# Kernel tuning notes

Hardware: AMD Instinct MI355X
Metric: run time of the kernel (lower is better)

Reference implementation:

```python
import jax, jax.numpy as jnp
import numpy as np

N, E, B = 50000, 800000, 64
F_IN, HID, H, L = 128, 128, 4, 4
C = HID // H  # per-head channels = 32
NEG_SLOPE = 0.2  # PyG GATConv default leaky_relu slope


def setup_inputs() -> dict:
    key = jax.random.key(0)
    ks = iter(jax.random.split(key, 32))
    rn = lambda shape, s=0.05: jax.random.normal(next(ks), shape, jnp.float32) * s
    x = jax.random.normal(next(ks), (N, F_IN), jnp.float32)
    edge_index = jax.random.randint(next(ks), (2, E), 0, N, jnp.int32)
    edge_attr = jax.random.uniform(next(ks), (E, 2), dtype=jnp.float32)
    batch = jnp.sort(jax.random.randint(next(ks), (N,), 0, B, jnp.int32))
    return {
        "x": x, "edge_attr": edge_attr,
        "Win": rn((F_IN, HID)), "b_in": jnp.zeros((HID,), jnp.float32),
        "We1": rn((2, 16)), "be1": jnp.zeros((16,), jnp.float32),
        "We2": rn((16, H)), "be2": jnp.zeros((H,), jnp.float32),
        "Wl": rn((L, HID, HID)), "a_src": rn((L, H, C)), "a_dst": rn((L, H, C)),
        "bl": jnp.zeros((L, HID), jnp.float32),
        "ln_g": jnp.ones((L, HID), jnp.float32), "ln_b": jnp.zeros((L, HID), jnp.float32),
        "Wg1": rn((HID, HID // 2)), "bg1": jnp.zeros((HID // 2,), jnp.float32),
        "Wg2": rn((HID // 2, 1)), "bg2": jnp.zeros((1,), jnp.float32),
        "edge_index": edge_index, "batch": batch,
    }


def _layer_norm(x, g, b, eps=1e-5):
    mu = x.mean(-1, keepdims=True)
    var = ((x - mu) ** 2).mean(-1, keepdims=True)
    return (x - mu) * jax.lax.rsqrt(var + eps) * g + b


def _gat_conv(h, src, dst, W, a_s, a_d, bias):
    # PyG GATConv (shared lin for src/dst), add_self_loops already in src/dst.
    xp = (h @ W).reshape(N, H, C)            # [N,H,C]
    as_n = (xp * a_s).sum(-1)                # [N,H]
    ad_n = (xp * a_d).sum(-1)                # [N,H]
    e = jax.nn.leaky_relu(as_n[src] + ad_n[dst], NEG_SLOPE)   # [E+N,H]
    m = jax.ops.segment_max(e, dst, num_segments=N)           # stable softmax per dst
    p = jnp.exp(e - m[dst])
    s = jax.ops.segment_sum(p, dst, num_segments=N)
    alpha = p / (s[dst] + 1e-16)
    out = jax.ops.segment_sum(xp[src] * alpha[..., None], dst, num_segments=N)
    return out.reshape(N, HID) + bias


def reference(x, edge_attr, Win, b_in, We1, be1, We2, be2, Wl, a_src, a_dst, bl,
              ln_g, ln_b, Wg1, bg1, Wg2, bg2, edge_index, batch):
    h = x @ Win + b_in                                   # input_proj
    # edge bias MLP -> per-edge scalar -> scatter_add crit_signal (no self loops)
    edge_bias = jax.nn.relu(edge_attr @ We1 + be1) @ We2 + be2   # [E,H]
    edge_scalar = edge_bias.mean(axis=1)                         # [E]
    crit = jnp.zeros((N,), h.dtype).at[edge_index[1]].add(edge_scalar)[:, None]
    # self loops for GATConv
    loop = jnp.arange(N, dtype=edge_index.dtype)
    src = jnp.concatenate([edge_index[0], loop])
    dst = jnp.concatenate([edge_index[1], loop])
    for i in range(L):  # fixed small layer count
        h_new = _gat_conv(h, src, dst, Wl[i], a_src[i], a_dst[i], bl[i])
        h_new = _layer_norm(h_new, ln_g[i], ln_b[i])
        h_new = h_new + crit                             # broadcast [N,1]
        h = h_new + h                                    # residual (shapes match); dropout=eval noop
    # GlobalAttention pooling: softmax(gate) over each graph, weighted sum
    gate = jnp.tanh(h @ Wg1 + bg1) @ Wg2 + bg2           # [N,1]
    gmax = jax.ops.segment_max(gate, batch, num_segments=B)
    gp = jnp.exp(gate - gmax[batch])
    gs = jax.ops.segment_sum(gp, batch, num_segments=B)
    gate_sm = gp / (gs[batch] + 1e-16)
    return jax.ops.segment_sum(gate_sm * h, batch, num_segments=B)   # [B,HID]
```

## Files before the change

kernel.cpp:

```cpp
#include <hip/hip_runtime.h>
#include <math.h>

#define N_NODES 50000
#define N_EDGES 800000
#define N_B     64

typedef __attribute__((ext_vector_type(8))) short v8s;
typedef __attribute__((ext_vector_type(4))) float v4f;
typedef __attribute__((ext_vector_type(2))) float v2f;

__device__ __forceinline__ float lrelu(float x){ return x > 0.f ? x : 0.2f*x; }
__device__ __forceinline__ unsigned short f2b(float f){
  unsigned u = __float_as_uint(f);
  return (unsigned short)((u + 0x7fffu + ((u >> 16) & 1u)) >> 16);
}
__device__ __forceinline__ float blo(unsigned u){ return __uint_as_float(u << 16); }
__device__ __forceinline__ float bhi(unsigned u){ return __uint_as_float(u & 0xffff0000u); }

__global__ void k_convsetup(const float* __restrict__ Win, const float* __restrict__ Wl,
                            const float* __restrict__ a_src, const float* __restrict__ a_dst,
                            const float* __restrict__ Wg1, const int* __restrict__ batch,
                            unsigned short* __restrict__ WinT, unsigned short* __restrict__ WlT,
                            unsigned short* __restrict__ Wg1T, int* __restrict__ start,
                            int* __restrict__ cnt){
  if (blockIdx.x >= 384){
    int i = (blockIdx.x - 384)*256 + threadIdx.x;
    if (i >= N_NODES) return;
    cnt[i] = 0;
    int b = batch[i];
    int bp = (i == 0) ? -1 : batch[i-1];
    for (int j = bp+1; j <= b; j++) start[j] = i;
    if (i == N_NODES-1){
      for (int j = b+1; j <= N_B; j++) start[j] = N_NODES;
    }
    return;
  }
  int i = blockIdx.x*256 + threadIdx.x;
  if (i < 16384){
    int n = i >> 7, k = i & 127;
    WinT[n*128+k] = f2b(Win[k*128+n]);
    return;
  }
  i -= 16384;
  if (i < 65536){
    int l = i >> 14, n = (i >> 7) & 127, k = i & 127;
    WlT[l*144*128 + n*128 + k] = f2b(Wl[l*16384 + k*128 + n]);
    return;
  }
  i -= 65536;
  if (i < 4096){
    int l = i >> 10, k = (i >> 3) & 127, t = i & 7;
    int hh = t & 3, sd = t >> 2;
    const float* av = (sd ? a_dst : a_src) + l*128 + hh*32;
    const float* wr = Wl + l*16384 + k*128 + hh*32;
    float s = 0.f;
    #pragma unroll
    for (int c = 0; c < 32; c++) s = fmaf(wr[c], av[c], s);
    WlT[l*144*128 + (128 + sd*4 + hh)*128 + k] = f2b(s);
    return;
  }
  i -= 4096;
  if (i < 4096){
    int l = i >> 10, r = (i >> 7) & 7, k = i & 127;
    WlT[l*144*128 + (136+r)*128 + k] = 0;
    return;
  }
  i -= 4096;
  if (i < 8192){
    int n = i >> 7, k = i & 127;
    Wg1T[n*128+k] = f2b(Wg1[k*64+n]);
  }
}

__global__ void k_hist(const int* __restrict__ ei, int* __restrict__ cnt, int* __restrict__ rank){
  int t = blockIdx.x*256 + threadIdx.x;
  if (t >= 200000) return;
  #pragma unroll
  for (int r = 0; r < 4; r++){
    int e = t + r*200000;
    int d = ei[N_EDGES + e];
    rank[e] = atomicAdd(&cnt[d], 1);
  }
}

__global__ void k_scan1(const int* __restrict__ cnt, int* __restrict__ incl, int* __restrict__ part){
  __shared__ int sh[256];
  int tid = threadIdx.x, i = blockIdx.x*256 + tid;
  int v = (i < N_NODES) ? cnt[i] : 0;
  sh[tid] = v; __syncthreads();
  for (int off = 1; off < 256; off <<= 1){
    int t = (tid >= off) ? sh[tid-off] : 0;
    __syncthreads();
    sh[tid] += t; __syncthreads();
  }
  if (i < N_NODES) incl[i] = sh[tid];
  if (tid == 255) part[blockIdx.x] = sh[255];
}
__global__ void k_scan23(const int* __restrict__ cnt, const int* __restrict__ incl,
                         const int* __restrict__ part, int* __restrict__ off){
  __shared__ int red[4];
  __shared__ int bsum;
  int tid = threadIdx.x, lane = tid & 63, wave = tid >> 6;
  int v = (tid < (int)blockIdx.x) ? part[tid] : 0;
  #pragma unroll
  for (int m = 1; m < 64; m <<= 1) v += __shfl_xor(v, m);
  if (lane == 0) red[wave] = v;
  __syncthreads();
  if (tid == 0) bsum = red[0]+red[1]+red[2]+red[3];
  __syncthreads();
  int i = blockIdx.x*256 + tid;
  if (i >= N_NODES) return;
  int e = incl[i] - cnt[i] + bsum;
  off[i] = e;
  if (i == N_NODES-1) off[N_NODES] = e + cnt[i];
}

__global__ void k_fill(const float* __restrict__ ea, const float* __restrict__ We1,
                       const float* __restrict__ be1, const float* __restrict__ We2,
                       const float* __restrict__ be2, const int* __restrict__ ei,
                       const int* __restrict__ off, const int* __restrict__ rank,
                       int2* __restrict__ es){
  __shared__ float w0[16], w1[16], bb[16], w2s[16];
  __shared__ float b2s;
  int tid = threadIdx.x;
  if (tid < 16){
    w0[tid] = We1[tid]; w1[tid] = We1[16+tid]; bb[tid] = be1[tid];
    w2s[tid] = 0.25f*(We2[tid*4]+We2[tid*4+1]+We2[tid*4+2]+We2[tid*4+3]);
  }
  if (tid == 0) b2s = 0.25f*(be2[0]+be2[1]+be2[2]+be2[3]);
  __syncthreads();
  int t = blockIdx.x*256 + tid;
  if (t >= 200000) return;
  #pragma unroll
  for (int r = 0; r < 4; r++){
    int e = t + r*200000;
    float a0 = ea[2*e], a1 = ea[2*e+1];
    float s = b2s;
    #pragma unroll
    for (int j = 0; j < 16; j++){
      float v = fmaf(a0, w0[j], fmaf(a1, w1[j], bb[j]));
      v = v > 0.f ? v : 0.f;
      s = fmaf(v, w2s[j], s);
    }
    int d = ei[N_EDGES + e];
    int p = off[d] + rank[e];
    es[p] = make_int2(ei[e], __float_as_int(s));
  }
}

template<int NT, int MODE>
__global__ __launch_bounds__(256) void k_mgemm(
    const float* __restrict__ A, const unsigned short* __restrict__ Bt,
    const float* __restrict__ bias,
    float* __restrict__ h,
    unsigned short* __restrict__ xpb, float* __restrict__ asn, float* __restrict__ adn,
    const float* __restrict__ Wg2, const float* __restrict__ bg2, float* __restrict__ gate)
{
  __shared__ __attribute__((aligned(16))) unsigned short Bs[NT*16][136];
  __shared__ __attribute__((aligned(16))) unsigned short As[4][16][136];
  int tid = threadIdx.x, wave = tid >> 6, lane = tid & 63;
  int l15 = lane & 15, quad = lane >> 4;
  int rbase = blockIdx.x * 64;
  for (int id = tid; id < NT*16*16; id += 256){
    int r = id >> 4, ch = id & 15;
    *(v8s*)&Bs[r][ch*8] = *(const v8s*)(Bt + r*128 + ch*8);
  }
  for (int id = tid; id < 64*16; id += 256){
    int r = id >> 4, ch = id & 15;
    int gr = rbase + r;
    v8s v = {0,0,0,0,0,0,0,0};
    if (gr < N_NODES){
      const float* Af = A + (size_t)gr*128 + ch*8;
      float4 va = *(const float4*)Af;
      float4 vb = *(const float4*)(Af + 4);
      v[0]=(short)f2b(va.x); v[1]=(short)f2b(va.y); v[2]=(short)f2b(va.z); v[3]=(short)f2b(va.w);
      v[4]=(short)f2b(vb.x); v[5]=(short)f2b(vb.y); v[6]=(short)f2b(vb.z); v[7]=(short)f2b(vb.w);
    }
    *(v8s*)&As[r >> 4][r & 15][ch*8] = v;
  }
  __syncthreads();
  v4f acc[NT];
  #pragma unroll
  for (int t = 0; t < NT; t++) acc[t] = (v4f){0.f,0.f,0.f,0.f};
  #pragma unroll
  for (int kb = 0; kb < 4; kb++){
    v8s a = *(v8s*)&As[wave][l15][kb*32 + quad*8];
    #pragma unroll
    for (int ct = 0; ct < NT; ct++){
      v8s b = *(v8s*)&Bs[ct*16 + l15][kb*32 + quad*8];
      acc[ct] = __builtin_amdgcn_mfma_f32_16x16x32_bf16(a, b, acc[ct], 0, 0, 0);
    }
  }
  int row0 = rbase + wave*16 + quad*4;
  if (MODE == 0){
    #pragma unroll
    for (int ct = 0; ct < 8; ct++){
      float bcol = bias[ct*16 + l15];
      #pragma unroll
      for (int r = 0; r < 4; r++){
        int gr = row0 + r;
        if (gr < N_NODES) h[(size_t)gr*128 + ct*16 + l15] = acc[ct][r] + bcol;
      }
    }
  } else if (MODE == 1){
    #pragma unroll
    for (int ct = 0; ct < 8; ct++){
      #pragma unroll
      for (int r = 0; r < 4; r++){
        int gr = row0 + r;
        if (gr < N_NODES) xpb[(size_t)gr*128 + ct*16 + l15] = f2b(acc[ct][r]);
      }
    }
    #pragma unroll
    for (int r = 0; r < 4; r++){
      int gr = row0 + r;
      if (gr < N_NODES){
        float v = acc[NT-1][r];
        if (l15 < 4) asn[gr*4 + l15] = v;
        else if (l15 < 8) adn[gr*4 + (l15-4)] = v;
      }
    }
  } else {
    float part[4] = {0.f,0.f,0.f,0.f};
    #pragma unroll
    for (int ct = 0; ct < NT; ct++){
      float b1 = bias[ct*16 + l15];
      float w2 = Wg2[ct*16 + l15];
      #pragma unroll
      for (int r = 0; r < 4; r++) part[r] = fmaf(tanhf(acc[ct][r] + b1), w2, part[r]);
    }
    #pragma unroll
    for (int m = 1; m < 16; m <<= 1){
      #pragma unroll
      for (int r = 0; r < 4; r++) part[r] += __shfl_xor(part[r], m);
    }
    if (l15 == 0){
      float b2 = bg2[0];
      #pragma unroll
      for (int r = 0; r < 4; r++){
        int gr = row0 + r;
        if (gr < N_NODES) gate[gr] = part[r] + b2;
      }
    }
  }
}

template<bool CRIT>
__global__ __launch_bounds__(256) void k_aggr(
    const unsigned short* __restrict__ xpb, const float* __restrict__ asn,
    const float* __restrict__ adn, const int* __restrict__ off,
    const int2* __restrict__ es,
    const float* __restrict__ bl, const float* __restrict__ lng,
    const float* __restrict__ lnb, float* __restrict__ crit,
    float* __restrict__ h)
{
  __shared__ float lp[4][256];
  int wave = threadIdx.x >> 6, lane = threadIdx.x & 63;
  int n = blockIdx.x*4 + wave;
  if (n >= N_NODES) return;
  int base = off[n], deg = off[n+1] - base;
  float4 ad4 = *(const float4*)(adn + n*4);
  float4 asf = *(const float4*)(asn + n*4);
  float ex = lrelu(asf.x+ad4.x), ey = lrelu(asf.y+ad4.y);
  float ez = lrelu(asf.z+ad4.z), ew = lrelu(asf.w+ad4.w);
  const unsigned* xw = (const unsigned*)xpb;
  float* myp = &lp[wave][0];
  int hh = lane >> 4;
  float cr, dsum = 0.f;
  v2f acc;
  unsigned us = (xw + ((size_t)(unsigned)n << 6))[lane];
  acc.x = blo(us); acc.y = bhi(us);

  if (deg <= 64){
    int sreg = 0;
    float cw = 0.f;
    float p0 = 0.f, p1 = 0.f, p2 = 0.f, p3 = 0.f;
    if (lane < deg){
      int2 er = es[base + lane];
      sreg = er.x;
      float4 a = *(const float4*)(asn + sreg*4);
      p0 = __expf(lrelu(a.x+ad4.x) - ex);
      p1 = __expf(lrelu(a.y+ad4.y) - ey);
      p2 = __expf(lrelu(a.z+ad4.z) - ez);
      p3 = __expf(lrelu(a.w+ad4.w) - ew);
      if (CRIT) cw = __int_as_float(er.y);
    }
    if (CRIT){
      #pragma unroll
      for (int m = 1; m < 64; m <<= 1) cw += __shfl_xor(cw, m);
      if (lane == 0) crit[n] = cw;
      cr = cw;
    } else cr = crit[n];
    *(float4*)(&myp[4*lane]) = make_float4(p0,p1,p2,p3);
    __threadfence_block();
    int degR = (deg + 7) & ~7;
    for (int c = 0; c < degR; c += 8){
      unsigned u[8];
      #pragma unroll
      for (int k = 0; k < 8; k++){
        int s0 = __builtin_amdgcn_readlane(sreg, c + k);
        u[k] = (xw + ((size_t)(unsigned)s0 << 6))[lane];
      }
      #pragma unroll
      for (int k = 0; k < 8; k++){
        float q = myp[4*(c+k) + hh];
        dsum += q;
        v2f v = {blo(u[k]), bhi(u[k])};
        acc += q * v;
      }
    }
    __threadfence_block();
  } else {
    if (CRIT){
      float cw = 0.f;
      for (int j = lane; j < deg; j += 64) cw += __int_as_float(es[base + j].y);
      #pragma unroll
      for (int m = 1; m < 64; m <<= 1) cw += __shfl_xor(cw, m);
      if (lane == 0) crit[n] = cw;
      cr = cw;
    } else cr = crit[n];
    for (int j0 = 0; j0 < deg; j0 += 64){
      int clen = deg - j0; if (clen > 64) clen = 64;
      int sreg = 0;
      float p0 = 0.f, p1 = 0.f, p2 = 0.f, p3 = 0.f;
      if (lane < clen){
        sreg = es[base + j0 + lane].x;
        float4 a = *(const float4*)(asn + sreg*4);
        p0 = __expf(lrelu(a.x+ad4.x) - ex);
        p1 = __expf(lrelu(a.y+ad4.y) - ey);
        p2 = __expf(lrelu(a.z+ad4.z) - ez);
        p3 = __expf(lrelu(a.w+ad4.w) - ew);
      }
      *(float4*)(&myp[4*lane]) = make_float4(p0,p1,p2,p3);
      __threadfence_block();
      int clenR = (clen + 7) & ~7;
      for (int c = 0; c < clenR; c += 8){
        unsigned u[8];
        #pragma unroll
        for (int k = 0; k < 8; k++){
          int s0 = __builtin_amdgcn_readlane(sreg, c + k);
          u[k] = (xw + ((size_t)(unsigned)s0 << 6))[lane];
        }
        #pragma unroll
        for (int k = 0; k < 8; k++){
          float q = myp[4*(c+k) + hh];
          dsum += q;
          v2f v = {blo(u[k]), bhi(u[k])};
          acc += q * v;
        }
      }
      __threadfence_block();
    }
  }
  float rden = 1.f / (dsum + 1.f + 1e-16f);
  int c0 = 2*lane;
  float2 blv = *(const float2*)(bl + c0);
  float o0 = acc.x*rden + blv.x;
  float o1 = acc.y*rden + blv.y;
  float su = o0 + o1, sq = o0*o0 + o1*o1;
  #pragma unroll
  for (int m = 1; m < 64; m <<= 1){ su += __shfl_xor(su, m); sq += __shfl_xor(sq, m); }
  float mu  = su * (1.f/128.f);
  float var = sq * (1.f/128.f) - mu*mu; var = var > 0.f ? var : 0.f;
  float inv = rsqrtf(var + 1e-5f);
  float2 rv  = *(const float2*)(h + (size_t)n*128 + c0);
  float2 gv  = *(const float2*)(lng + c0);
  float2 bv2 = *(const float2*)(lnb + c0);
  o0 = (o0-mu)*inv*gv.x + bv2.x + cr + rv.x;
  o1 = (o1-mu)*inv*gv.y + bv2.y + cr + rv.y;
  *(float2*)(&h[(size_t)n*128 + c0]) = make_float2(o0, o1);
}

__global__ __launch_bounds__(256) void k_pool(
    const float* __restrict__ h, float* __restrict__ gate,
    const int* __restrict__ start, float* __restrict__ out)
{
  __shared__ float red[4];
  __shared__ float sbc;
  __shared__ float4 accs[8][32];
  int b = blockIdx.x;
  int s0 = start[b], s1 = start[b+1];
  int tid = threadIdx.x, lane = tid & 63, wave = tid >> 6;
  float m = -3.0e38f;
  for (int i = s0 + tid; i < s1; i += 256) m = fmaxf(m, gate[i]);
  #pragma unroll
  for (int k = 1; k < 64; k <<= 1) m = fmaxf(m, __shfl_xor(m, k));
  if (lane == 0) red[wave] = m;
  __syncthreads();
  if (tid == 0) sbc = fmaxf(fmaxf(red[0],red[1]), fmaxf(red[2],red[3]));
  __syncthreads();
  float gm = sbc;
  __syncthreads();
  float s = 0.f;
  for (int i = s0 + tid; i < s1; i += 256){
    float p = __expf(gate[i] - gm);
    gate[i] = p;
    s += p;
  }
  #pragma unroll
  for (int k = 1; k < 64; k <<= 1) s += __shfl_xor(s, k);
  if (lane == 0) red[wave] = s;
  __syncthreads();
  if (tid == 0) sbc = red[0]+red[1]+red[2]+red[3];
  __syncthreads();
  float inv = 1.f / (sbc + 1e-16f);
  int c4 = (tid & 31) * 4;
  int g  = tid >> 5;
  float4 acc = make_float4(0.f,0.f,0.f,0.f);
  for (int i = s0 + g; i < s1; i += 8){
    float p = gate[i];
    float4 hv = *(const float4*)(h + (size_t)i*128 + c4);
    acc.x = fmaf(p,hv.x,acc.x); acc.y = fmaf(p,hv.y,acc.y);
    acc.z = fmaf(p,hv.z,acc.z); acc.w = fmaf(p,hv.w,acc.w);
  }
  accs[g][tid & 31] = acc;
  __syncthreads();
  if (g == 0){
    float4 t = acc;
    #pragma unroll
    for (int k = 1; k < 8; k++){
      float4 o = accs[k][tid & 31];
      t.x += o.x; t.y += o.y; t.z += o.z; t.w += o.w;
    }
    t.x *= inv; t.y *= inv; t.z *= inv; t.w *= inv;
    *(float4*)(out + b*128 + c4) = t;
  }
}

extern "C" void kernel_launch(void* const* d_in, const int* in_sizes, int n_in,
                              void* d_out, int out_size, void* d_ws, size_t ws_size,
                              hipStream_t stream){
  (void)in_sizes; (void)n_in; (void)out_size; (void)ws_size;
  const float* x    = (const float*)d_in[0];
  const float* ea   = (const float*)d_in[1];
  const float* Win  = (const float*)d_in[2];
  const float* b_in = (const float*)d_in[3];
  const float* We1  = (const float*)d_in[4];
  const float* be1  = (const float*)d_in[5];
  const float* We2  = (const float*)d_in[6];
  const float* be2  = (const float*)d_in[7];
  const float* Wl   = (const float*)d_in[8];
  const float* a_src= (const float*)d_in[9];
  const float* a_dst= (const float*)d_in[10];
  const float* bl   = (const float*)d_in[11];
  const float* lng  = (const float*)d_in[12];
  const float* lnb  = (const float*)d_in[13];
  const float* Wg1  = (const float*)d_in[14];
  const float* bg1  = (const float*)d_in[15];
  const float* Wg2  = (const float*)d_in[16];
  const float* bg2  = (const float*)d_in[17];
  const int*   ei   = (const int*)d_in[18];
  const int*   batch= (const int*)d_in[19];
  float* out = (float*)d_out;

  char* w = (char*)d_ws;
  auto alloc = [&](size_t bytes){ char* p = w; w += (bytes + 255) & ~(size_t)255; return p; };
  float* h    = (float*)alloc((size_t)N_NODES*128*4);
  unsigned short* xpb = (unsigned short*)alloc((size_t)N_NODES*128*2);
  float* asn  = (float*)alloc((size_t)N_NODES*4*4);
  float* adn  = (float*)alloc((size_t)N_NODES*4*4);
  float* crit = (float*)alloc((size_t)N_NODES*4);
  int*   cnt  = (int*)alloc((size_t)N_NODES*4);
  int*   incl = (int*)alloc((size_t)N_NODES*4);
  int*   part = (int*)alloc(256*4);
  int*   off  = (int*)alloc((size_t)(N_NODES+1)*4);
  int*   rank = (int*)alloc((size_t)N_EDGES*4);
  int2*  es   = (int2*)alloc((size_t)N_EDGES*8);
  float* gate = (float*)alloc((size_t)N_NODES*4);
  int*   start= (int*)alloc((size_t)(N_B+1)*4);
  unsigned short* WinT = (unsigned short*)alloc((size_t)128*128*2);
  unsigned short* WlT  = (unsigned short*)alloc((size_t)4*144*128*2);
  unsigned short* Wg1T = (unsigned short*)alloc((size_t)64*128*2);

  int nb_n = (N_NODES + 255)/256;
  int nb_w = (N_NODES + 3)/4;
  int nb_g = (N_NODES + 63)/64;
  int nb_cs = 384 + nb_n;
  int nb_4e = (200000 + 255)/256;

  k_convsetup<<<nb_cs,256,0,stream>>>(Win, Wl, a_src, a_dst, Wg1, batch,
                                      WinT, WlT, Wg1T, start, cnt);
  k_hist<<<nb_4e,256,0,stream>>>(ei, cnt, rank);
  k_mgemm<8,0><<<nb_g,256,0,stream>>>(x, WinT, b_in, h,
                                      nullptr, nullptr, nullptr, nullptr, nullptr, nullptr);
  k_scan1<<<nb_n,256,0,stream>>>(cnt, incl, part);
  k_scan23<<<nb_n,256,0,stream>>>(cnt, incl, part, off);
  k_fill<<<nb_4e,256,0,stream>>>(ea, We1, be1, We2, be2, ei, off, rank, es);
  for (int l = 0; l < 4; l++){
    k_mgemm<9,1><<<nb_g,256,0,stream>>>(h, WlT + (size_t)l*144*128, nullptr, nullptr,
                                        xpb, asn, adn, nullptr, nullptr, nullptr);
    if (l == 0)
      k_aggr<true><<<nb_w,256,0,stream>>>(xpb, asn, adn, off, es,
                                          bl + l*128, lng + l*128, lnb + l*128, crit, h);
    else
      k_aggr<false><<<nb_w,256,0,stream>>>(xpb, asn, adn, off, es,
                                           bl + l*128, lng + l*128, lnb + l*128, crit, h);
  }
  k_mgemm<4,2><<<nb_g,256,0,stream>>>(h, Wg1T, bg1, nullptr,
                                      nullptr, nullptr, nullptr, Wg2, bg2, gate);
  k_pool<<<N_B,256,0,stream>>>(h, gate, start, out);
}
```

Baseline: 440.1 us.

## Split pooling across four blocks per graph, widen edge loops and gather batches

```diff
diff --git a/kernel.cpp b/kernel.cpp
--- a/kernel.cpp
+++ b/kernel.cpp
@@ -22,11 +22,12 @@
                             const float* __restrict__ Wg1, const int* __restrict__ batch,
                             unsigned short* __restrict__ WinT, unsigned short* __restrict__ WlT,
                             unsigned short* __restrict__ Wg1T, int* __restrict__ start,
-                            int* __restrict__ cnt){
+                            int* __restrict__ cnt, float* __restrict__ out){
   if (blockIdx.x >= 384){
     int i = (blockIdx.x - 384)*256 + threadIdx.x;
     if (i >= N_NODES) return;
     cnt[i] = 0;
+    if (i < N_B*128) out[i] = 0.f;
     int b = batch[i];
     int bp = (i == 0) ? -1 : batch[i-1];
     for (int j = bp+1; j <= b; j++) start[j] = i;
@@ -74,10 +75,10 @@
 
 __global__ void k_hist(const int* __restrict__ ei, int* __restrict__ cnt, int* __restrict__ rank){
   int t = blockIdx.x*256 + threadIdx.x;
-  if (t >= 200000) return;
-  #pragma unroll
-  for (int r = 0; r < 4; r++){
-    int e = t + r*200000;
+  if (t >= 100000) return;
+  #pragma unroll
+  for (int r = 0; r < 8; r++){
+    int e = t + r*100000;
     int d = ei[N_EDGES + e];
     rank[e] = atomicAdd(&cnt[d], 1);
   }
@@ -130,10 +131,10 @@
   if (tid == 0) b2s = 0.25f*(be2[0]+be2[1]+be2[2]+be2[3]);
   __syncthreads();
   int t = blockIdx.x*256 + tid;
-  if (t >= 200000) return;
-  #pragma unroll
-  for (int r = 0; r < 4; r++){
-    int e = t + r*200000;
+  if (t >= 100000) return;
+  #pragma unroll
+  for (int r = 0; r < 8; r++){
+    int e = t + r*100000;
     float a0 = ea[2*e], a1 = ea[2*e+1];
     float s = b2s;
     #pragma unroll
@@ -293,16 +294,16 @@
     } else cr = crit[n];
     *(float4*)(&myp[4*lane]) = make_float4(p0,p1,p2,p3);
     __threadfence_block();
-    int degR = (deg + 7) & ~7;
-    for (int c = 0; c < degR; c += 8){
-      unsigned u[8];
-      #pragma unroll
-      for (int k = 0; k < 8; k++){
+    int degR = ((deg + 11) / 12) * 12;
+    for (int c = 0; c < degR; c += 12){
+      unsigned u[12];
+      #pragma unroll
+      for (int k = 0; k < 12; k++){
         int s0 = __builtin_amdgcn_readlane(sreg, c + k);
         u[k] = (xw + ((size_t)(unsigned)s0 << 6))[lane];
       }
       #pragma unroll
-      for (int k = 0; k < 8; k++){
+      for (int k = 0; k < 12; k++){
         float q = myp[4*(c+k) + hh];
         dsum += q;
         v2f v = {blo(u[k]), bhi(u[k])};
@@ -372,13 +373,13 @@
 }
 
 __global__ __launch_bounds__(256) void k_pool(
-    const float* __restrict__ h, float* __restrict__ gate,
+    const float* __restrict__ h, const float* __restrict__ gate,
     const int* __restrict__ start, float* __restrict__ out)
 {
   __shared__ float red[4];
   __shared__ float sbc;
   __shared__ float4 accs[8][32];
-  int b = blockIdx.x;
+  int b = blockIdx.x >> 2, quarter = blockIdx.x & 3;
   int s0 = start[b], s1 = start[b+1];
   int tid = threadIdx.x, lane = tid & 63, wave = tid >> 6;
   float m = -3.0e38f;
@@ -392,11 +393,7 @@
   float gm = sbc;
   __syncthreads();
   float s = 0.f;
-  for (int i = s0 + tid; i < s1; i += 256){
-    float p = __expf(gate[i] - gm);
-    gate[i] = p;
-    s += p;
-  }
+  for (int i = s0 + tid; i < s1; i += 256) s += __expf(gate[i] - gm);
   #pragma unroll
   for (int k = 1; k < 64; k <<= 1) s += __shfl_xor(s, k);
   if (lane == 0) red[wave] = s;
@@ -407,8 +404,8 @@
   int c4 = (tid & 31) * 4;
   int g  = tid >> 5;
   float4 acc = make_float4(0.f,0.f,0.f,0.f);
-  for (int i = s0 + g; i < s1; i += 8){
-    float p = gate[i];
+  for (int i = s0 + quarter*8 + g; i < s1; i += 32){
+    float p = __expf(gate[i] - gm);
     float4 hv = *(const float4*)(h + (size_t)i*128 + c4);
     acc.x = fmaf(p,hv.x,acc.x); acc.y = fmaf(p,hv.y,acc.y);
     acc.z = fmaf(p,hv.z,acc.z); acc.w = fmaf(p,hv.w,acc.w);
@@ -422,8 +419,10 @@
       float4 o = accs[k][tid & 31];
       t.x += o.x; t.y += o.y; t.z += o.z; t.w += o.w;
     }
-    t.x *= inv; t.y *= inv; t.z *= inv; t.w *= inv;
-    *(float4*)(out + b*128 + c4) = t;
+    atomicAdd(out + b*128 + c4 + 0, t.x*inv);
+    atomicAdd(out + b*128 + c4 + 1, t.y*inv);
+    atomicAdd(out + b*128 + c4 + 2, t.z*inv);
+    atomicAdd(out + b*128 + c4 + 3, t.w*inv);
   }
 }
 
@@ -476,16 +475,16 @@
   int nb_w = (N_NODES + 3)/4;
   int nb_g = (N_NODES + 63)/64;
   int nb_cs = 384 + nb_n;
-  int nb_4e = (200000 + 255)/256;
+  int nb_8e = (100000 + 255)/256;
 
   k_convsetup<<<nb_cs,256,0,stream>>>(Win, Wl, a_src, a_dst, Wg1, batch,
-                                      WinT, WlT, Wg1T, start, cnt);
-  k_hist<<<nb_4e,256,0,stream>>>(ei, cnt, rank);
+                                      WinT, WlT, Wg1T, start, cnt, out);
+  k_hist<<<nb_8e,256,0,stream>>>(ei, cnt, rank);
   k_mgemm<8,0><<<nb_g,256,0,stream>>>(x, WinT, b_in, h,
                                       nullptr, nullptr, nullptr, nullptr, nullptr, nullptr);
   k_scan1<<<nb_n,256,0,stream>>>(cnt, incl, part);
   k_scan23<<<nb_n,256,0,stream>>>(cnt, incl, part, off);
-  k_fill<<<nb_4e,256,0,stream>>>(ea, We1, be1, We2, be2, ei, off, rank, es);
+  k_fill<<<nb_8e,256,0,stream>>>(ea, We1, be1, We2, be2, ei, off, rank, es);
   for (int l = 0; l < 4; l++){
     k_mgemm<9,1><<<nb_g,256,0,stream>>>(h, WlT + (size_t)l*144*128, nullptr, nullptr,
                                         xpb, asn, adn, nullptr, nullptr, nullptr);
@@ -498,5 +497,5 @@
   }
   k_mgemm<4,2><<<nb_g,256,0,stream>>>(h, Wg1T, bg1, nullptr,
                                       nullptr, nullptr, nullptr, Wg2, bg2, gate);
-  k_pool<<<N_B,256,0,stream>>>(h, gate, start, out);
-}
+  k_pool<<<N_B*4,256,0,stream>>>(h, gate, start, out);
+}
```

Result: faster. 428.5 us (-2.6%).
